# Kernel tuning notes

Measured on AMD Instinct MI355X. Metric: run time of the kernel, lower is better.

The kernel has to match this reference:

```python
import jax, jax.numpy as jnp
import numpy as np

D_IN = 1024
D_OUT = 1024


def setup_inputs() -> dict:
    key = jax.random.key(0)
    kx, kq, kk, kv = jax.random.split(key, 4)
    s = 1.0 / np.sqrt(D_IN)
    x = jax.random.normal(kx, (2, 4096, D_IN), dtype=jnp.float32)
    # nn.Linear weights: shape [d_out, d_in], y = x @ W.T (no bias)
    W_query = jax.random.normal(kq, (D_OUT, D_IN), dtype=jnp.float32) * s
    W_key = jax.random.normal(kk, (D_OUT, D_IN), dtype=jnp.float32) * s
    W_value = jax.random.normal(kv, (D_OUT, D_IN), dtype=jnp.float32) * s
    return {"x": x, "W_query": W_query, "W_key": W_key, "W_value": W_value}


def reference(x, W_query, W_key, W_value):
    # QKV projections: [b, n, d_in] @ [d_in, d_out]
    q = jnp.einsum('bnd,od->bno', x, W_query)
    k = jnp.einsum('bnd,od->bno', x, W_key)
    v = jnp.einsum('bnd,od->bno', x, W_value)
    d_k = k.shape[-1]
    scores = jnp.einsum('bqo,bko->bqk', q, k) / jnp.sqrt(jnp.asarray(d_k, x.dtype))
    # NOTE: source applies no causal mask despite the class name
    attn = jax.nn.softmax(scores, axis=-1)
    return jnp.einsum('bqk,bko->bqo', attn, v)
```

## Files before the change

kernel.cpp:

```cpp
#include <hip/hip_runtime.h>
#include <hip/hip_bf16.h>
#include <hip/hip_fp16.h>
#include <stdint.h>

typedef __bf16 bf16_t;
typedef __bf16 bf16x8 __attribute__((ext_vector_type(8)));
typedef float f32x4 __attribute__((ext_vector_type(4)));

typedef __attribute__((address_space(1))) void gv_t;
typedef __attribute__((address_space(3))) void lv_t;

__device__ inline unsigned short f2bf_bits(float f) {
  uint32_t u = __float_as_uint(f);
  u += 0x7FFFu + ((u >> 16) & 1u);
  return (unsigned short)(u >> 16);
}
__device__ inline bf16_t f2bf(float f) {
  unsigned short h = f2bf_bits(f);
  return __builtin_bit_cast(bf16_t, h);
}

__device__ inline void storeC(float* p, float v) { *p = v; }
__device__ inline void storeC(bf16_t* p, float v) { *p = f2bf(v); }
__device__ inline void storeC(__half* p, float v) { *p = __float2half(v); }

__global__ __launch_bounds__(256)
void convert_all(const float* __restrict__ x, const float* __restrict__ wq,
                 const float* __restrict__ wk, const float* __restrict__ wv,
                 bf16_t* __restrict__ xb, bf16_t* __restrict__ wqkb,
                 bf16_t* __restrict__ wvb)
{
  const int64_t NX = 8192LL * 1024, NW = 1024LL * 1024;
  const int64_t total4 = (NX + 3 * NW) >> 2;
  for (int64_t i = (int64_t)blockIdx.x * blockDim.x + threadIdx.x; i < total4;
       i += (int64_t)gridDim.x * blockDim.x) {
    int64_t e = i << 2;
    const float* src; bf16_t* dst; int64_t off;
    if (e < NX)               { src = x;  dst = xb;         off = e; }
    else if (e < NX + NW)     { src = wq; dst = wqkb;       off = e - NX; }
    else if (e < NX + 2 * NW) { src = wk; dst = wqkb + NW;  off = e - NX - NW; }
    else                      { src = wv; dst = wvb;        off = e - NX - 2 * NW; }
    float4 f = *(const float4*)(src + off);
    uint32_t lo = ((uint32_t)f2bf_bits(f.y) << 16) | f2bf_bits(f.x);
    uint32_t hi = ((uint32_t)f2bf_bits(f.w) << 16) | f2bf_bits(f.z);
    *(uint2*)(dst + off) = make_uint2(lo, hi);
  }
}

template <typename OUT_T, typename OUT2_T>
__global__ __launch_bounds__(256, 2)
void gemm128(const bf16_t* __restrict__ A, const bf16_t* __restrict__ B,
             OUT_T* __restrict__ C0, OUT2_T* __restrict__ C1,
             int K, int lda, int ldb, int ldc,
             int64_t b_batch_stride, int bm_per_batch,
             int64_t za_off, int64_t zb_off)
{
  __shared__ bf16_t As[2][128][64];
  __shared__ bf16_t Bs[2][128][64];

  const int tid  = threadIdx.x;
  const int wid  = tid >> 6;
  const int lane = tid & 63;
  const int wm = wid >> 1;
  const int wn = wid & 1;
  const int64_t bm = blockIdx.x;
  const int64_t bn = blockIdx.y;
  const int z = blockIdx.z;

  const bf16_t* Ap = A + (int64_t)z * za_off;
  const bf16_t* Bp = B + (bm / bm_per_batch) * b_batch_stride
                       + (int64_t)z * zb_off;

  const int srow  = tid >> 3;
  const int sslot = (tid & 7) ^ (srow & 7);
  const int64_t lda64 = lda, ldb64 = ldb;
  const bf16_t* Ag = Ap + (bm * 128 + srow) * lda64 + sslot * 8;
  const bf16_t* Bg = Bp + (bn * 128 + srow) * ldb64 + sslot * 8;

  auto stageA = [&](int buf, int t, int q) {
    const bf16_t* src = Ag + (int64_t)(q * 32) * lda64 + t * 64;
    char* dst = (char*)&As[buf][0][0] + (q * 32 + wid * 8) * 128;
    __builtin_amdgcn_global_load_lds((const gv_t*)src, (lv_t*)dst, 16, 0, 0);
  };
  auto stageB = [&](int buf, int t, int q) {
    const bf16_t* src = Bg + (int64_t)(q * 32) * ldb64 + t * 64;
    char* dst = (char*)&Bs[buf][0][0] + (q * 32 + wid * 8) * 128;
    __builtin_amdgcn_global_load_lds((const gv_t*)src, (lv_t*)dst, 16, 0, 0);
  };

  const int frow   = lane & 15;
  const int fcol16 = lane >> 4;
  const int xorv   = (lane & 7) << 4;
  const int ck0 = (fcol16 * 16) ^ xorv;
  const int ck1 = (64 + fcol16 * 16) ^ xorv;
  const int arowb = (wm * 64 + frow) * 128;
  const int browb = (wn * 64 + frow) * 128;

  f32x4 acc[4][4];
  #pragma unroll
  for (int m = 0; m < 4; m++)
    #pragma unroll
    for (int n = 0; n < 4; n++) acc[m][n] = f32x4{0.f, 0.f, 0.f, 0.f};

  const int NT = K >> 6;

  stageA(0, 0, 0); stageA(0, 0, 1); stageA(0, 0, 2); stageA(0, 0, 3);
  stageB(0, 0, 0); stageB(0, 0, 1); stageB(0, 0, 2); stageB(0, 0, 3);
  asm volatile("s_waitcnt vmcnt(0)" ::: "memory");
  __builtin_amdgcn_s_barrier();
  __builtin_amdgcn_sched_barrier(0);

  bf16x8 a[4][2], bb[4][2];

  for (int g = 0; g < NT; ++g) {
    const int buf = g & 1;
    const char* lA = (const char*)&As[buf][0][0];
    const char* lB = (const char*)&Bs[buf][0][0];

    #pragma unroll
    for (int m = 0; m < 4; m++)
      a[m][0] = *(const bf16x8*)(lA + arowb + m * 2048 + ck0);
    #pragma unroll
    for (int n = 0; n < 4; n++)
      bb[n][0] = *(const bf16x8*)(lB + browb + n * 2048 + ck0);
    #pragma unroll
    for (int m = 0; m < 4; m++)
      a[m][1] = *(const bf16x8*)(lA + arowb + m * 2048 + ck1);
    #pragma unroll
    for (int n = 0; n < 4; n++)
      bb[n][1] = *(const bf16x8*)(lB + browb + n * 2048 + ck1);

    if (g + 1 < NT) {
      stageA(buf ^ 1, g + 1, 0); stageA(buf ^ 1, g + 1, 1);
      stageA(buf ^ 1, g + 1, 2); stageA(buf ^ 1, g + 1, 3);
      stageB(buf ^ 1, g + 1, 0); stageB(buf ^ 1, g + 1, 1);
      stageB(buf ^ 1, g + 1, 2); stageB(buf ^ 1, g + 1, 3);
    }

    __builtin_amdgcn_s_setprio(1);
    #pragma unroll
    for (int k = 0; k < 2; k++)
      #pragma unroll
      for (int m = 0; m < 4; m++)
        #pragma unroll
        for (int n = 0; n < 4; n++)
          acc[m][n] = __builtin_amdgcn_mfma_f32_16x16x32_bf16(
              a[m][k], bb[n][k], acc[m][n], 0, 0, 0);
    __builtin_amdgcn_s_setprio(0);

    asm volatile("s_waitcnt vmcnt(0)" ::: "memory");
    __builtin_amdgcn_s_barrier();
    __builtin_amdgcn_sched_barrier(0);
  }

  const int crow = (lane >> 4) * 4;
  const int ccol = lane & 15;
  if (z == 0) {
    #pragma unroll
    for (int m = 0; m < 4; m++)
      #pragma unroll
      for (int n = 0; n < 4; n++)
        #pragma unroll
        for (int j = 0; j < 4; j++) {
          int64_t row = bm * 128 + wm * 64 + m * 16 + crow + j;
          int64_t col = bn * 128 + wn * 64 + n * 16 + ccol;
          storeC(&C0[row * (int64_t)ldc + col], acc[m][n][j]);
        }
  } else {
    #pragma unroll
    for (int m = 0; m < 4; m++)
      #pragma unroll
      for (int n = 0; n < 4; n++)
        #pragma unroll
        for (int j = 0; j < 4; j++) {
          int64_t row = bm * 128 + wm * 64 + m * 16 + crow + j;
          int64_t col = bn * 128 + wn * 64 + n * 16 + ccol;
          storeC(&C1[row * (int64_t)ldc + col], acc[m][n][j]);
        }
  }
}

template <typename OUT_T, typename OUT2_T>
__global__ __launch_bounds__(256, 1)
void gemm_fat(const bf16_t* __restrict__ A, const bf16_t* __restrict__ B,
              OUT_T* __restrict__ C0, OUT2_T* __restrict__ C1,
              int K, int lda, int ldb, int ldc,
              int64_t b_batch_stride, int bm_per_batch,
              int64_t za_off, int64_t zb_off)
{
  __shared__ bf16_t As[2][256][64];
  __shared__ bf16_t Bs[2][256][64];

  const int tid  = threadIdx.x;
  const int wid  = tid >> 6;
  const int lane = tid & 63;
  const int wm = wid >> 1;
  const int wn = wid & 1;
  const int64_t bm = blockIdx.x;
  const int64_t bn = blockIdx.y;
  const int z = blockIdx.z;

  const bf16_t* Ap = A + (int64_t)z * za_off;
  const bf16_t* Bp = B + (bm / bm_per_batch) * b_batch_stride
                       + (int64_t)z * zb_off;

  const int srow  = tid >> 3;
  const int sslot = (tid & 7) ^ (srow & 7);
  const int64_t lda64 = lda, ldb64 = ldb;
  const bf16_t* Ag = Ap + (bm * 256 + srow) * lda64 + sslot * 8;
  const bf16_t* Bg = Bp + (bn * 256 + srow) * ldb64 + sslot * 8;

  auto stageA = [&](int buf, int t, int q) {
    const bf16_t* src = Ag + (int64_t)(q * 32) * lda64 + t * 64;
    char* dst = (char*)&As[buf][0][0] + (q * 32 + wid * 8) * 128;
    __builtin_amdgcn_global_load_lds((const gv_t*)src, (lv_t*)dst, 16, 0, 0);
  };
  auto stageB = [&](int buf, int t, int q) {
    const bf16_t* src = Bg + (int64_t)(q * 32) * ldb64 + t * 64;
    char* dst = (char*)&Bs[buf][0][0] + (q * 32 + wid * 8) * 128;
    __builtin_amdgcn_global_load_lds((const gv_t*)src, (lv_t*)dst, 16, 0, 0);
  };

  const int frow   = lane & 15;
  const int fcol16 = lane >> 4;
  const int xorv   = (lane & 7) << 4;
  const int ck0 = (fcol16 * 16) ^ xorv;
  const int ck1 = (64 + fcol16 * 16) ^ xorv;
  const int arowb = (wm * 128 + frow) * 128;
  const int browb = (wn * 128 + frow) * 128;

  f32x4 acc[8][8];
  #pragma unroll
  for (int m = 0; m < 8; m++)
    #pragma unroll
    for (int n = 0; n < 8; n++) acc[m][n] = f32x4{0.f, 0.f, 0.f, 0.f};

  const int NT = K >> 6;

  #pragma unroll
  for (int q = 0; q < 8; q++) stageA(0, 0, q);
  #pragma unroll
  for (int q = 0; q < 8; q++) stageB(0, 0, q);
  asm volatile("s_waitcnt vmcnt(0)" ::: "memory");
  __builtin_amdgcn_s_barrier();
  __builtin_amdgcn_sched_barrier(0);

  bf16x8 a[8][2], bb[8][2];

  for (int g = 0; g < NT; ++g) {
    const int buf = g & 1;
    const char* lA = (const char*)&As[buf][0][0];
    const char* lB = (const char*)&Bs[buf][0][0];

    #pragma unroll
    for (int m = 0; m < 8; m++)
      a[m][0] = *(const bf16x8*)(lA + arowb + m * 2048 + ck0);
    #pragma unroll
    for (int n = 0; n < 8; n++)
      bb[n][0] = *(const bf16x8*)(lB + browb + n * 2048 + ck0);
    #pragma unroll
    for (int m = 0; m < 8; m++)
      a[m][1] = *(const bf16x8*)(lA + arowb + m * 2048 + ck1);
    #pragma unroll
    for (int n = 0; n < 8; n++)
      bb[n][1] = *(const bf16x8*)(lB + browb + n * 2048 + ck1);

    if (g + 1 < NT) {
      #pragma unroll
      for (int q = 0; q < 8; q++) stageA(buf ^ 1, g + 1, q);
      #pragma unroll
      for (int q = 0; q < 8; q++) stageB(buf ^ 1, g + 1, q);
    }

    __builtin_amdgcn_s_setprio(1);
    #pragma unroll
    for (int k = 0; k < 2; k++)
      #pragma unroll
      for (int m = 0; m < 8; m++)
        #pragma unroll
        for (int n = 0; n < 8; n++)
          acc[m][n] = __builtin_amdgcn_mfma_f32_16x16x32_bf16(
              a[m][k], bb[n][k], acc[m][n], 0, 0, 0);
    __builtin_amdgcn_s_setprio(0);

    asm volatile("s_waitcnt vmcnt(0)" ::: "memory");
    __builtin_amdgcn_s_barrier();
    __builtin_amdgcn_sched_barrier(0);
  }

  const int crow = (lane >> 4) * 4;
  const int ccol = lane & 15;
  if (z == 0) {
    #pragma unroll
    for (int m = 0; m < 8; m++)
      #pragma unroll
      for (int n = 0; n < 8; n++)
        #pragma unroll
        for (int j = 0; j < 4; j++) {
          int64_t row = bm * 256 + wm * 128 + m * 16 + crow + j;
          int64_t col = bn * 256 + wn * 128 + n * 16 + ccol;
          storeC(&C0[row * (int64_t)ldc + col], acc[m][n][j]);
        }
  } else {
    #pragma unroll
    for (int m = 0; m < 8; m++)
      #pragma unroll
      for (int n = 0; n < 8; n++)
        #pragma unroll
        for (int j = 0; j < 4; j++) {
          int64_t row = bm * 256 + wm * 128 + m * 16 + crow + j;
          int64_t col = bn * 256 + wn * 128 + n * 16 + ccol;
          storeC(&C1[row * (int64_t)ldc + col], acc[m][n][j]);
        }
  }
}

__global__ __launch_bounds__(256)
void softmax_rows(__half* __restrict__ SP)
{
  const int64_t row = blockIdx.x;
  __half* s = SP + row * 4096;
  bf16_t* p = (bf16_t*)s;
  const int tid = threadIdx.x;
  const float scale = 0.03125f;

  float v[16];
  float vmax = -3.4e38f;
  #pragma unroll
  for (int i = 0; i < 4; i++) {
    uint2 raw = *(const uint2*)(s + i * 1024 + tid * 4);
    __half2 h01 = __builtin_bit_cast(__half2, raw.x);
    __half2 h23 = __builtin_bit_cast(__half2, raw.y);
    float2 f01 = __half22float2(h01);
    float2 f23 = __half22float2(h23);
    v[i * 4 + 0] = f01.x * scale;
    v[i * 4 + 1] = f01.y * scale;
    v[i * 4 + 2] = f23.x * scale;
    v[i * 4 + 3] = f23.y * scale;
    vmax = fmaxf(vmax, fmaxf(fmaxf(v[i*4+0], v[i*4+1]),
                             fmaxf(v[i*4+2], v[i*4+3])));
  }
  #pragma unroll
  for (int o = 32; o > 0; o >>= 1) vmax = fmaxf(vmax, __shfl_xor(vmax, o));
  __shared__ float redm[4];
  __shared__ float reds[4];
  if ((tid & 63) == 0) redm[tid >> 6] = vmax;
  __syncthreads();
  vmax = fmaxf(fmaxf(redm[0], redm[1]), fmaxf(redm[2], redm[3]));

  float lsum = 0.f;
  #pragma unroll
  for (int i = 0; i < 16; i++) {
    v[i] = __expf(v[i] - vmax);
    lsum += v[i];
  }
  #pragma unroll
  for (int o = 32; o > 0; o >>= 1) lsum += __shfl_xor(lsum, o);
  if ((tid & 63) == 0) reds[tid >> 6] = lsum;
  __syncthreads();
  lsum = (reds[0] + reds[1]) + (reds[2] + reds[3]);
  const float inv = 1.0f / lsum;

  #pragma unroll
  for (int i = 0; i < 4; i++) {
    uint32_t lo = ((uint32_t)f2bf_bits(v[i*4+1] * inv) << 16) | f2bf_bits(v[i*4+0] * inv);
    uint32_t hi = ((uint32_t)f2bf_bits(v[i*4+3] * inv) << 16) | f2bf_bits(v[i*4+2] * inv);
    *(uint2*)(p + i * 1024 + tid * 4) = make_uint2(lo, hi);
  }
}

__global__ __launch_bounds__(256)
void addk_h4(float4* __restrict__ o, const uint2* __restrict__ a, int64_t n4)
{
  for (int64_t i = (int64_t)blockIdx.x * blockDim.x + threadIdx.x; i < n4;
       i += (int64_t)gridDim.x * blockDim.x) {
    float4 x = o[i];
    uint2 raw = a[i];
    __half2 h01 = __builtin_bit_cast(__half2, raw.x);
    __half2 h23 = __builtin_bit_cast(__half2, raw.y);
    float2 f01 = __half22float2(h01);
    float2 f23 = __half22float2(h23);
    x.x += f01.x; x.y += f01.y; x.z += f23.x; x.w += f23.y;
    o[i] = x;
  }
}

extern "C" void kernel_launch(void* const* d_in, const int* in_sizes, int n_in,
                              void* d_out, int out_size, void* d_ws, size_t ws_size,
                              hipStream_t stream) {
  const float* x  = (const float*)d_in[0];
  const float* wq = (const float*)d_in[1];
  const float* wk = (const float*)d_in[2];
  const float* wv = (const float*)d_in[3];
  float* out = (float*)d_out;

  char* ws = (char*)d_ws;
  bf16_t* xb   = (bf16_t*)ws;
  bf16_t* wqkb = (bf16_t*)(ws + (16LL << 20));
  bf16_t* wvb  = (bf16_t*)(ws + (20LL << 20));
  __half* S    = (__half*)ws;
  bf16_t* qk   = (bf16_t*)(ws + (64LL << 20));
  __half* pk16 = (__half*)(ws + (64LL << 20));
  bf16_t* vt   = (bf16_t*)(ws + (96LL << 20));

  const int NO_BATCH = 1 << 30;

  convert_all<<<2048, 256, 0, stream>>>(x, wq, wk, wv, xb, wqkb, wvb);

  gemm_fat<bf16_t, bf16_t><<<dim3(32, 8, 1), 256, 0, stream>>>(
      xb, wqkb, qk, qk, 1024, 1024, 1024, 2048, 0, NO_BATCH, 0, 0);

  gemm128<bf16_t, bf16_t><<<dim3(8, 64, 1), 256, 0, stream>>>(
      wvb, xb, vt, vt, 1024, 1024, 1024, 8192, 0, NO_BATCH, 0, 0);

  gemm_fat<__half, __half><<<dim3(32, 16, 1), 256, 0, stream>>>(
      qk, qk + 1024, S, S, 1024, 2048, 2048, 4096, 4096LL * 2048, 16, 0, 0);

  softmax_rows<<<8192, 256, 0, stream>>>(S);

  gemm_fat<float, __half><<<dim3(32, 4, 2), 256, 0, stream>>>(
      (const bf16_t*)S, vt, out, pk16, 2048, 4096, 8192, 1024,
      4096, 16, 2048, 2048);

  addk_h4<<<2048, 256, 0, stream>>>((float4*)out, (const uint2*)pk16,
                                    8192LL * 1024 / 4);
}
```

Baseline: 244.5 us.

## Replace fat GEMMs with 512-thread 256-tile kernel, XCD remap, drop split-K

```diff
diff --git a/kernel.cpp b/kernel.cpp
--- a/kernel.cpp
+++ b/kernel.cpp
@@ -23,6 +23,16 @@
 __device__ inline void storeC(float* p, float v) { *p = v; }
 __device__ inline void storeC(bf16_t* p, float v) { *p = f2bf(v); }
 __device__ inline void storeC(__half* p, float v) { *p = __float2half(v); }
+
+__device__ inline void xcd_remap(int64_t& bm, int64_t& bn) {
+  const int gx  = gridDim.x;
+  const int h   = blockIdx.x + gx * blockIdx.y;
+  const int gpx = gx >> 3;
+  const int xcd = h & 7;
+  const int s   = h >> 3;
+  bm = xcd * gpx + (s % gpx);
+  bn = s / gpx;
+}
 
 __global__ __launch_bounds__(256)
 void convert_all(const float* __restrict__ x, const float* __restrict__ wq,
@@ -47,6 +57,229 @@
   }
 }
 
+template <typename OUT_T>
+__global__ __launch_bounds__(256)
+void gemm_bt(const bf16_t* __restrict__ A, const bf16_t* __restrict__ B,
+             OUT_T* __restrict__ C, int K, int lda, int ldb, int ldc,
+             int64_t b_batch_stride, int bm_per_batch)
+{
+  __shared__ bf16_t As[2][128 * 32];
+  __shared__ bf16_t Bs[2][128 * 32];
+  const int tid  = threadIdx.x;
+  const int wid  = tid >> 6;
+  const int lane = tid & 63;
+  const int wm = wid >> 1, wn = wid & 1;
+  const int64_t bm = blockIdx.x;
+  const int64_t bn = blockIdx.y;
+
+  const bf16_t* Bb = B + (bm / bm_per_batch) * b_batch_stride;
+
+  const int c0row = (wid * 2 + 0) * 16 + (lane >> 2);
+  const int c1row = (wid * 2 + 1) * 16 + (lane >> 2);
+  const int scol  = (lane & 3) * 8;
+
+  const bf16_t* Ar0 = A  + (bm * 128 + c0row) * lda + scol;
+  const bf16_t* Ar1 = A  + (bm * 128 + c1row) * lda + scol;
+  const bf16_t* Br0 = Bb + (bn * 128 + c0row) * ldb + scol;
+  const bf16_t* Br1 = Bb + (bn * 128 + c1row) * ldb + scol;
+
+  const int ad0 = (wid * 2 + 0) * 512;
+  const int ad1 = (wid * 2 + 1) * 512;
+
+  const int frow = lane & 15;
+  const int fk   = (lane >> 4) * 8;
+  const int aoff = (wm * 64 + frow) * 32 + fk;
+  const int boff = (wn * 64 + frow) * 32 + fk;
+
+  f32x4 acc[4][4];
+  #pragma unroll
+  for (int m = 0; m < 4; m++)
+    #pragma unroll
+    for (int n = 0; n < 4; n++) acc[m][n] = f32x4{0.f, 0.f, 0.f, 0.f};
+
+  auto stage = [&](int buf, int k0) {
+    __builtin_amdgcn_global_load_lds((const gv_t*)(Ar0 + k0),
+                                     (lv_t*)(&As[buf][ad0]), 16, 0, 0);
+    __builtin_amdgcn_global_load_lds((const gv_t*)(Ar1 + k0),
+                                     (lv_t*)(&As[buf][ad1]), 16, 0, 0);
+    __builtin_amdgcn_global_load_lds((const gv_t*)(Br0 + k0),
+                                     (lv_t*)(&Bs[buf][ad0]), 16, 0, 0);
+    __builtin_amdgcn_global_load_lds((const gv_t*)(Br1 + k0),
+                                     (lv_t*)(&Bs[buf][ad1]), 16, 0, 0);
+  };
+
+  stage(0, 0);
+  __syncthreads();
+  int cur = 0;
+  for (int k0 = 0; k0 < K; k0 += 32) {
+    if (k0 + 32 < K) stage(cur ^ 1, k0 + 32);
+
+    bf16x8 af[4], bfr[4];
+    #pragma unroll
+    for (int m = 0; m < 4; m++)
+      af[m] = *(const bf16x8*)(&As[cur][aoff + m * 16 * 32]);
+    #pragma unroll
+    for (int n = 0; n < 4; n++)
+      bfr[n] = *(const bf16x8*)(&Bs[cur][boff + n * 16 * 32]);
+    #pragma unroll
+    for (int m = 0; m < 4; m++)
+      #pragma unroll
+      for (int n = 0; n < 4; n++)
+        acc[m][n] = __builtin_amdgcn_mfma_f32_16x16x32_bf16(af[m], bfr[n],
+                                                            acc[m][n], 0, 0, 0);
+    __syncthreads();
+    cur ^= 1;
+  }
+
+  const int crow = (lane >> 4) * 4;
+  const int ccol = lane & 15;
+  #pragma unroll
+  for (int m = 0; m < 4; m++)
+    #pragma unroll
+    for (int n = 0; n < 4; n++)
+      #pragma unroll
+      for (int j = 0; j < 4; j++) {
+        int64_t row = bm * 128 + wm * 64 + m * 16 + crow + j;
+        int64_t col = bn * 128 + wn * 64 + n * 16 + ccol;
+        storeC(&C[row * ldc + col], acc[m][n][j]);
+      }
+}
+
+template <typename OUT_T, typename OUT2_T>
+__global__ __launch_bounds__(512, 2)
+void gemm256(const bf16_t* __restrict__ A, const bf16_t* __restrict__ B,
+             OUT_T* __restrict__ C0, OUT2_T* __restrict__ C1,
+             int K, int lda, int ldb, int ldc,
+             int64_t b_batch_stride, int bm_per_batch,
+             int64_t za_off, int64_t zb_off)
+{
+  __shared__ bf16_t As[2][256][64];
+  __shared__ bf16_t Bs[2][256][64];
+
+  const int tid  = threadIdx.x;
+  const int wid  = tid >> 6;
+  const int lane = tid & 63;
+  const int wm = wid >> 2;
+  const int wn = wid & 3;
+  int64_t bm, bn;
+  xcd_remap(bm, bn);
+  const int z = blockIdx.z;
+
+  const bf16_t* Ap = A + (int64_t)z * za_off;
+  const bf16_t* Bp = B + (bm / bm_per_batch) * b_batch_stride
+                       + (int64_t)z * zb_off;
+
+  const int srow  = tid >> 3;
+  const int sslot = (tid & 7) ^ (srow & 7);
+  const int64_t lda64 = lda, ldb64 = ldb;
+  const bf16_t* Ag = Ap + (bm * 256 + srow) * lda64 + sslot * 8;
+  const bf16_t* Bg = Bp + (bn * 256 + srow) * ldb64 + sslot * 8;
+
+  auto stageA = [&](int buf, int t, int q) {
+    const bf16_t* src = Ag + (int64_t)(q * 64) * lda64 + t * 64;
+    char* dst = (char*)&As[buf][0][0] + (q * 64 + wid * 8) * 128;
+    __builtin_amdgcn_global_load_lds((const gv_t*)src, (lv_t*)dst, 16, 0, 0);
+  };
+  auto stageB = [&](int buf, int t, int q) {
+    const bf16_t* src = Bg + (int64_t)(q * 64) * ldb64 + t * 64;
+    char* dst = (char*)&Bs[buf][0][0] + (q * 64 + wid * 8) * 128;
+    __builtin_amdgcn_global_load_lds((const gv_t*)src, (lv_t*)dst, 16, 0, 0);
+  };
+
+  const int frow   = lane & 15;
+  const int fcol16 = lane >> 4;
+  const int xorv   = (lane & 7) << 4;
+  const int ck0 = (fcol16 * 16) ^ xorv;
+  const int ck1 = (64 + fcol16 * 16) ^ xorv;
+  const int arowb = (wm * 128 + frow) * 128;
+  const int browb = (wn * 64  + frow) * 128;
+
+  f32x4 acc[8][4];
+  #pragma unroll
+  for (int m = 0; m < 8; m++)
+    #pragma unroll
+    for (int n = 0; n < 4; n++) acc[m][n] = f32x4{0.f, 0.f, 0.f, 0.f};
+
+  const int NT = K >> 6;
+
+  #pragma unroll
+  for (int q = 0; q < 4; q++) stageA(0, 0, q);
+  #pragma unroll
+  for (int q = 0; q < 4; q++) stageB(0, 0, q);
+  asm volatile("s_waitcnt vmcnt(0)" ::: "memory");
+  __builtin_amdgcn_s_barrier();
+  __builtin_amdgcn_sched_barrier(0);
+
+  bf16x8 a[8][2], bb[4][2];
+
+  for (int g = 0; g < NT; ++g) {
+    const int buf = g & 1;
+    const char* lA = (const char*)&As[buf][0][0];
+    const char* lB = (const char*)&Bs[buf][0][0];
+
+    #pragma unroll
+    for (int m = 0; m < 8; m++)
+      a[m][0] = *(const bf16x8*)(lA + arowb + m * 2048 + ck0);
+    #pragma unroll
+    for (int n = 0; n < 4; n++)
+      bb[n][0] = *(const bf16x8*)(lB + browb + n * 2048 + ck0);
+    #pragma unroll
+    for (int m = 0; m < 8; m++)
+      a[m][1] = *(const bf16x8*)(lA + arowb + m * 2048 + ck1);
+    #pragma unroll
+    for (int n = 0; n < 4; n++)
+      bb[n][1] = *(const bf16x8*)(lB + browb + n * 2048 + ck1);
+
+    if (g + 1 < NT) {
+      #pragma unroll
+      for (int q = 0; q < 4; q++) stageA(buf ^ 1, g + 1, q);
+      #pragma unroll
+      for (int q = 0; q < 4; q++) stageB(buf ^ 1, g + 1, q);
+    }
+
+    __builtin_amdgcn_s_setprio(1);
+    #pragma unroll
+    for (int k = 0; k < 2; k++)
+      #pragma unroll
+      for (int m = 0; m < 8; m++)
+        #pragma unroll
+        for (int n = 0; n < 4; n++)
+          acc[m][n] = __builtin_amdgcn_mfma_f32_16x16x32_bf16(
+              a[m][k], bb[n][k], acc[m][n], 0, 0, 0);
+    __builtin_amdgcn_s_setprio(0);
+
+    asm volatile("s_waitcnt vmcnt(0)" ::: "memory");
+    __builtin_amdgcn_s_barrier();
+    __builtin_amdgcn_sched_barrier(0);
+  }
+
+  const int crow = (lane >> 4) * 4;
+  const int ccol = lane & 15;
+  if (z == 0) {
+    #pragma unroll
+    for (int m = 0; m < 8; m++)
+      #pragma unroll
+      for (int n = 0; n < 4; n++)
+        #pragma unroll
+        for (int j = 0; j < 4; j++) {
+          int64_t row = bm * 256 + wm * 128 + m * 16 + crow + j;
+          int64_t col = bn * 256 + wn * 64 + n * 16 + ccol;
+          storeC(&C0[row * (int64_t)ldc + col], acc[m][n][j]);
+        }
+  } else {
+    #pragma unroll
+    for (int m = 0; m < 8; m++)
+      #pragma unroll
+      for (int n = 0; n < 4; n++)
+        #pragma unroll
+        for (int j = 0; j < 4; j++) {
+          int64_t row = bm * 256 + wm * 128 + m * 16 + crow + j;
+          int64_t col = bn * 256 + wn * 64 + n * 16 + ccol;
+          storeC(&C1[row * (int64_t)ldc + col], acc[m][n][j]);
+        }
+  }
+}
+
 template <typename OUT_T, typename OUT2_T>
 __global__ __launch_bounds__(256, 2)
 void gemm128(const bf16_t* __restrict__ A, const bf16_t* __restrict__ B,
@@ -63,8 +296,8 @@
   const int lane = tid & 63;
   const int wm = wid >> 1;
   const int wn = wid & 1;
-  const int64_t bm = blockIdx.x;
-  const int64_t bn = blockIdx.y;
+  int64_t bm, bn;
+  xcd_remap(bm, bn);
   const int z = blockIdx.z;
 
   const bf16_t* Ap = A + (int64_t)z * za_off;
@@ -175,141 +408,6 @@
         for (int j = 0; j < 4; j++) {
           int64_t row = bm * 128 + wm * 64 + m * 16 + crow + j;
           int64_t col = bn * 128 + wn * 64 + n * 16 + ccol;
-          storeC(&C1[row * (int64_t)ldc + col], acc[m][n][j]);
-        }
-  }
-}
-
-template <typename OUT_T, typename OUT2_T>
-__global__ __launch_bounds__(256, 1)
-void gemm_fat(const bf16_t* __restrict__ A, const bf16_t* __restrict__ B,
-              OUT_T* __restrict__ C0, OUT2_T* __restrict__ C1,
-              int K, int lda, int ldb, int ldc,
-              int64_t b_batch_stride, int bm_per_batch,
-              int64_t za_off, int64_t zb_off)
-{
-  __shared__ bf16_t As[2][256][64];
-  __shared__ bf16_t Bs[2][256][64];
-
-  const int tid  = threadIdx.x;
-  const int wid  = tid >> 6;
-  const int lane = tid & 63;
-  const int wm = wid >> 1;
-  const int wn = wid & 1;
-  const int64_t bm = blockIdx.x;
-  const int64_t bn = blockIdx.y;
-  const int z = blockIdx.z;
-
-  const bf16_t* Ap = A + (int64_t)z * za_off;
-  const bf16_t* Bp = B + (bm / bm_per_batch) * b_batch_stride
-                       + (int64_t)z * zb_off;
-
-  const int srow  = tid >> 3;
-  const int sslot = (tid & 7) ^ (srow & 7);
-  const int64_t lda64 = lda, ldb64 = ldb;
-  const bf16_t* Ag = Ap + (bm * 256 + srow) * lda64 + sslot * 8;
-  const bf16_t* Bg = Bp + (bn * 256 + srow) * ldb64 + sslot * 8;
-
-  auto stageA = [&](int buf, int t, int q) {
-    const bf16_t* src = Ag + (int64_t)(q * 32) * lda64 + t * 64;
-    char* dst = (char*)&As[buf][0][0] + (q * 32 + wid * 8) * 128;
-    __builtin_amdgcn_global_load_lds((const gv_t*)src, (lv_t*)dst, 16, 0, 0);
-  };
-  auto stageB = [&](int buf, int t, int q) {
-    const bf16_t* src = Bg + (int64_t)(q * 32) * ldb64 + t * 64;
-    char* dst = (char*)&Bs[buf][0][0] + (q * 32 + wid * 8) * 128;
-    __builtin_amdgcn_global_load_lds((const gv_t*)src, (lv_t*)dst, 16, 0, 0);
-  };
-
-  const int frow   = lane & 15;
-  const int fcol16 = lane >> 4;
-  const int xorv   = (lane & 7) << 4;
-  const int ck0 = (fcol16 * 16) ^ xorv;
-  const int ck1 = (64 + fcol16 * 16) ^ xorv;
-  const int arowb = (wm * 128 + frow) * 128;
-  const int browb = (wn * 128 + frow) * 128;
-
-  f32x4 acc[8][8];
-  #pragma unroll
-  for (int m = 0; m < 8; m++)
-    #pragma unroll
-    for (int n = 0; n < 8; n++) acc[m][n] = f32x4{0.f, 0.f, 0.f, 0.f};
-
-  const int NT = K >> 6;
-
-  #pragma unroll
-  for (int q = 0; q < 8; q++) stageA(0, 0, q);
-  #pragma unroll
-  for (int q = 0; q < 8; q++) stageB(0, 0, q);
-  asm volatile("s_waitcnt vmcnt(0)" ::: "memory");
-  __builtin_amdgcn_s_barrier();
-  __builtin_amdgcn_sched_barrier(0);
-
-  bf16x8 a[8][2], bb[8][2];
-
-  for (int g = 0; g < NT; ++g) {
-    const int buf = g & 1;
-    const char* lA = (const char*)&As[buf][0][0];
-    const char* lB = (const char*)&Bs[buf][0][0];
-
-    #pragma unroll
-    for (int m = 0; m < 8; m++)
-      a[m][0] = *(const bf16x8*)(lA + arowb + m * 2048 + ck0);
-    #pragma unroll
-    for (int n = 0; n < 8; n++)
-      bb[n][0] = *(const bf16x8*)(lB + browb + n * 2048 + ck0);
-    #pragma unroll
-    for (int m = 0; m < 8; m++)
-      a[m][1] = *(const bf16x8*)(lA + arowb + m * 2048 + ck1);
-    #pragma unroll
-    for (int n = 0; n < 8; n++)
-      bb[n][1] = *(const bf16x8*)(lB + browb + n * 2048 + ck1);
-
-    if (g + 1 < NT) {
-      #pragma unroll
-      for (int q = 0; q < 8; q++) stageA(buf ^ 1, g + 1, q);
-      #pragma unroll
-      for (int q = 0; q < 8; q++) stageB(buf ^ 1, g + 1, q);
-    }
-
-    __builtin_amdgcn_s_setprio(1);
-    #pragma unroll
-    for (int k = 0; k < 2; k++)
-      #pragma unroll
-      for (int m = 0; m < 8; m++)
-        #pragma unroll
-        for (int n = 0; n < 8; n++)
-          acc[m][n] = __builtin_amdgcn_mfma_f32_16x16x32_bf16(
-              a[m][k], bb[n][k], acc[m][n], 0, 0, 0);
-    __builtin_amdgcn_s_setprio(0);
-
-    asm volatile("s_waitcnt vmcnt(0)" ::: "memory");
-    __builtin_amdgcn_s_barrier();
-    __builtin_amdgcn_sched_barrier(0);
-  }
-
-  const int crow = (lane >> 4) * 4;
-  const int ccol = lane & 15;
-  if (z == 0) {
-    #pragma unroll
-    for (int m = 0; m < 8; m++)
-      #pragma unroll
-      for (int n = 0; n < 8; n++)
-        #pragma unroll
-        for (int j = 0; j < 4; j++) {
-          int64_t row = bm * 256 + wm * 128 + m * 16 + crow + j;
-          int64_t col = bn * 256 + wn * 128 + n * 16 + ccol;
-          storeC(&C0[row * (int64_t)ldc + col], acc[m][n][j]);
-        }
-  } else {
-    #pragma unroll
-    for (int m = 0; m < 8; m++)
-      #pragma unroll
-      for (int n = 0; n < 8; n++)
-        #pragma unroll
-        for (int j = 0; j < 4; j++) {
-          int64_t row = bm * 256 + wm * 128 + m * 16 + crow + j;
-          int64_t col = bn * 256 + wn * 128 + n * 16 + ccol;
           storeC(&C1[row * (int64_t)ldc + col], acc[m][n][j]);
         }
   }
@@ -369,22 +467,6 @@
   }
 }
 
-__global__ __launch_bounds__(256)
-void addk_h4(float4* __restrict__ o, const uint2* __restrict__ a, int64_t n4)
-{
-  for (int64_t i = (int64_t)blockIdx.x * blockDim.x + threadIdx.x; i < n4;
-       i += (int64_t)gridDim.x * blockDim.x) {
-    float4 x = o[i];
-    uint2 raw = a[i];
-    __half2 h01 = __builtin_bit_cast(__half2, raw.x);
-    __half2 h23 = __builtin_bit_cast(__half2, raw.y);
-    float2 f01 = __half22float2(h01);
-    float2 f23 = __half22float2(h23);
-    x.x += f01.x; x.y += f01.y; x.z += f23.x; x.w += f23.y;
-    o[i] = x;
-  }
-}
-
 extern "C" void kernel_launch(void* const* d_in, const int* in_sizes, int n_in,
                               void* d_out, int out_size, void* d_ws, size_t ws_size,
                               hipStream_t stream) {
@@ -400,28 +482,24 @@
   bf16_t* wvb  = (bf16_t*)(ws + (20LL << 20));
   __half* S    = (__half*)ws;
   bf16_t* qk   = (bf16_t*)(ws + (64LL << 20));
-  __half* pk16 = (__half*)(ws + (64LL << 20));
   bf16_t* vt   = (bf16_t*)(ws + (96LL << 20));
 
   const int NO_BATCH = 1 << 30;
 
   convert_all<<<2048, 256, 0, stream>>>(x, wq, wk, wv, xb, wqkb, wvb);
 
-  gemm_fat<bf16_t, bf16_t><<<dim3(32, 8, 1), 256, 0, stream>>>(
+  gemm256<bf16_t, bf16_t><<<dim3(32, 8, 1), 512, 0, stream>>>(
       xb, wqkb, qk, qk, 1024, 1024, 1024, 2048, 0, NO_BATCH, 0, 0);
 
-  gemm128<bf16_t, bf16_t><<<dim3(8, 64, 1), 256, 0, stream>>>(
-      wvb, xb, vt, vt, 1024, 1024, 1024, 8192, 0, NO_BATCH, 0, 0);
-
-  gemm_fat<__half, __half><<<dim3(32, 16, 1), 256, 0, stream>>>(
+  gemm_bt<bf16_t><<<dim3(8, 64), 256, 0, stream>>>(
+      wvb, xb, vt, 1024, 1024, 1024, 8192, 0, NO_BATCH);
+
+  gemm256<__half, __half><<<dim3(32, 16, 1), 512, 0, stream>>>(
       qk, qk + 1024, S, S, 1024, 2048, 2048, 4096, 4096LL * 2048, 16, 0, 0);
 
   softmax_rows<<<8192, 256, 0, stream>>>(S);
 
-  gemm_fat<float, __half><<<dim3(32, 4, 2), 256, 0, stream>>>(
-      (const bf16_t*)S, vt, out, pk16, 2048, 4096, 8192, 1024,
-      4096, 16, 2048, 2048);
-
-  addk_h4<<<2048, 256, 0, stream>>>((float4*)out, (const uint2*)pk16,
-                                    8192LL * 1024 / 4);
-}
+  gemm128<float, float><<<dim3(64, 8, 1), 256, 0, stream>>>(
+      (const bf16_t*)S, vt, out, out, 4096, 4096, 8192, 1024,
+      4096, 32, 0, 0);
+}
```

Result: faster. 217.1 us, median of 2 (-11.2%).
